# Optimization experiments

Hardware: AMD Instinct MI355X
Metric: run time of the kernel (lower is better)

Reference implementation:

```python
import jax, jax.numpy as jnp
import numpy as np

ALPHAS = [2.0 ** k for k in range(-3, 2)]  # default GaussianKernel bandwidth magnitudes


def _cdist(x, y):
    # Euclidean distance matrix with torch.cdist-compatible zero-distance subgradient.
    sq = (jnp.sum(x * x, axis=1)[:, None]
          + jnp.sum(y * y, axis=1)[None, :]
          - 2.0 * (x @ y.T))
    sq = jnp.maximum(sq, 0.0)
    safe = jnp.where(sq > 0, sq, 1.0)
    return jnp.where(sq > 0, jnp.sqrt(safe), 0.0)


def setup_inputs() -> dict:
    key = jax.random.key(0)
    k1, k2 = jax.random.split(key)
    xs = jax.random.normal(k1, (4096, 256), dtype=jnp.float32)
    xt = jax.random.normal(k2, (4096, 256), dtype=jnp.float32)
    return {"xs": xs, "xt": xt}


def reference(xs, xt):
    xs = xs.reshape(xs.shape[0], -1)
    xt = xt.reshape(xt.shape[0], -1)
    b = xs.shape[0]

    # Compute the three pairwise distance matrices ONCE (the torch loop redoes
    # this per kernel; the math is identical).
    dxx = _cdist(xs, xs)  # [B, B]
    dyy = _cdist(xt, xt)
    dxy = _cdist(xs, xt)

    # sigma^2 = alpha * mean(dist), with the mean detached (stop_gradient).
    mxx = jax.lax.stop_gradient(jnp.mean(dxx))
    myy = jax.lax.stop_gradient(jnp.mean(dyy))
    mxy = jax.lax.stop_gradient(jnp.mean(dxy))

    total = jnp.zeros_like(dxx)
    for a in ALPHAS:
        kxx = jnp.exp(-dxx / (2.0 * a * mxx))
        kyy = jnp.exp(-dyy / (2.0 * a * myy))
        kxy = jnp.exp(-dxy / (2.0 * a * mxy))
        total = total + (kxx + kyy - 2.0 * kxy)

    loss = jnp.sqrt(jnp.sum(total) / (b * (b - 1.0)))
    return jnp.where(jnp.isnan(loss), jnp.zeros_like(loss), loss)
```

## Files before the change

### kernel.cpp

```cpp
#include <hip/hip_runtime.h>

#define BN 4096
#define KD 256
#define TILE 256
#define BK 64

typedef short bf16x8 __attribute__((ext_vector_type(8)));
typedef float f32x4 __attribute__((ext_vector_type(4)));
typedef unsigned short ushort_t;
typedef unsigned int uint_t;

#define NSLOT 528

__device__ inline void async_load16(const void* g, void* l) {
    __builtin_amdgcn_global_load_lds((const __attribute__((address_space(1))) void*)g,
                                     (__attribute__((address_space(3))) void*)l,
                                     16, 0, 0);
}

__device__ inline ushort_t f2bf(float f) {
    union { float f; unsigned int u; } x;
    x.f = f;
    unsigned int u = x.u;
    unsigned int r = (u + 0x7fffu + ((u >> 16) & 1u)) >> 16;
    return (ushort_t)r;
}

__device__ __forceinline__ float fast_sqrt(float x) {
    return __builtin_amdgcn_sqrtf(x);
}
__device__ __forceinline__ float fast_exp2(float x) {
    return __builtin_amdgcn_exp2f(x);
}

__device__ __forceinline__ void decode_slot(int slot, int& z, int& bi, int& bj) {
    if (slot >= 272) {
        z = 2; int t = slot - 272; bi = t >> 4; bj = t & 15;
    } else {
        z = (slot >= 136) ? 1 : 0;
        int t = slot - z * 136;
        int b = (int)(16.5f - sqrtf(272.25f - 2.0f * (float)t));
        while (b * (33 - b) / 2 > t) --b;
        while ((b + 1) * (32 - b) / 2 <= t) ++b;
        bi = b;
        bj = bi + (t - bi * (33 - bi) / 2);
    }
}

__global__ __launch_bounds__(256) void norm_cvt(
        const float* __restrict__ xs, const float* __restrict__ xt,
        ushort_t* __restrict__ xsb, ushort_t* __restrict__ xtb,
        float* __restrict__ norms) {
    int w = threadIdx.x >> 6;
    int lane = threadIdx.x & 63;
    int row = blockIdx.x * 4 + w;
    const float* src = (row < BN) ? xs + (size_t)row * KD
                                  : xt + (size_t)(row - BN) * KD;
    ushort_t* dst = (row < BN) ? xsb + (size_t)row * KD
                               : xtb + (size_t)(row - BN) * KD;
    float4 v = ((const float4*)src)[lane];
    float s = v.x * v.x + v.y * v.y + v.z * v.z + v.w * v.w;
#pragma unroll
    for (int off = 32; off > 0; off >>= 1) s += __shfl_xor(s, off, 64);
    if (lane == 0) norms[row] = s;
    ushort4 o;
    o.x = f2bf(v.x); o.y = f2bf(v.y); o.z = f2bf(v.z); o.w = f2bf(v.w);
    ((ushort4*)dst)[lane] = o;
}


template <int PASS>
__global__ __launch_bounds__(512, 1) void mmd_gemm(
        const ushort_t* __restrict__ xsb, const ushort_t* __restrict__ xtb,
        const float* __restrict__ norms,
        const float* __restrict__ p1, float* __restrict__ pout) {
    const int slot = blockIdx.x;
    int z, bi, bj;
    decode_slot(slot, z, bi, bj);

    const ushort_t* X = (z == 1) ? xtb : xsb;
    const ushort_t* Y = (z == 0) ? xsb : xtb;
    const float* nX = norms + ((z == 1) ? BN : 0);
    const float* nY = norms + ((z == 0) ? 0 : BN);

    const int tid = threadIdx.x;
    const int lane = tid & 63;
    const int w = tid >> 6;
    const int wr = w >> 2;
    const int wc = w & 3;
    const int m16 = lane & 15;
    const int q = lane >> 4;

    const int i0 = bi * TILE;
    const int j0 = bj * TILE;

    __shared__ ushort_t sm[2][2][TILE * BK];
    __shared__ float red[8];
    __shared__ double rs[8][3];

    float nhb = 0.0f;
    if (PASS == 2) {
        double a0 = 0.0, a1 = 0.0, a2 = 0.0;
        for (int s = tid; s < NSLOT; s += 512) {
            double v = (double)p1[s];
            if (s < 136) a0 += v; else if (s < 272) a1 += v; else a2 += v;
        }
#pragma unroll
        for (int off = 32; off > 0; off >>= 1) {
            a0 += __shfl_xor(a0, off, 64);
            a1 += __shfl_xor(a1, off, 64);
            a2 += __shfl_xor(a2, off, 64);
        }
        if (lane == 0) { rs[w][0] = a0; rs[w][1] = a1; rs[w][2] = a2; }
        __syncthreads();
        double sz = 0.0;
#pragma unroll
        for (int ww = 0; ww < 8; ++ww) sz += rs[ww][z];
        double mz = sz * (1.0 / 16777216.0);
        nhb = (float)(-1.4426950408889634 / (4.0 * mz));
    }

    const int rbase = tid >> 3;
    const int gc = (tid & 7) ^ (rbase & 7);
    const uint_t offA = ((uint_t)(i0 + rbase) * KD + (uint_t)gc * 8) * 2u;
    const uint_t offB = ((uint_t)(j0 + rbase) * KD + (uint_t)gc * 8) * 2u;
    const char* Xc = (const char*)X;
    const char* Yc = (const char*)Y;

    f32x4 acc[8][4] = {};

    auto stage = [&](int kt, int p) {
        const uint_t kb = (uint_t)(kt * BK * 2);
        char* ldsA = (char*)&sm[p][0][0] + tid * 16;
        char* ldsB = (char*)&sm[p][1][0] + tid * 16;
#pragma unroll
        for (int t = 0; t < 4; ++t) {
            const uint_t rowoff = (uint_t)(t * 64 * KD * 2);
            async_load16(Xc + (offA + rowoff + kb), ldsA + t * 8192);
            async_load16(Yc + (offB + rowoff + kb), ldsB + t * 8192);
        }
    };

    auto compute = [&](int p) {
#pragma unroll
        for (int ks = 0; ks < 2; ++ks) {
            const int kap = ks * 4 + q;
            const int pos = kap ^ (m16 & 7);
            bf16x8 bfv[4];
#pragma unroll
            for (int ng = 0; ng < 4; ++ng)
                bfv[ng] = *(const bf16x8*)&sm[p][1][(wc * 64 + ng * 16 + m16) * BK + pos * 8];
#pragma unroll
            for (int rg = 0; rg < 8; ++rg) {
                bf16x8 a = *(const bf16x8*)&sm[p][0][(wr * 128 + rg * 16 + m16) * BK + pos * 8];
#pragma unroll
                for (int ng = 0; ng < 4; ++ng)
                    acc[rg][ng] = __builtin_amdgcn_mfma_f32_16x16x32_bf16(
                        a, bfv[ng], acc[rg][ng], 0, 0, 0);
            }
        }
    };

    stage(0, 0);
#pragma unroll
    for (int t = 0; t < 4; ++t) {
        const int p = t & 1;
        if (t < 3) {
            stage(t + 1, p ^ 1);
            asm volatile("s_waitcnt vmcnt(8)" ::: "memory");
        } else {
            asm volatile("s_waitcnt vmcnt(0)" ::: "memory");
        }
        __builtin_amdgcn_s_barrier();
        compute(p);
        if (t < 3) __builtin_amdgcn_s_barrier();
    }

    float nyv[4];
#pragma unroll
    for (int ng = 0; ng < 4; ++ng)
        nyv[ng] = nY[j0 + wc * 64 + ng * 16 + m16];

    const bool diag = (z < 2 && bi == bj);
    float local = 0.0f;
#pragma unroll
    for (int rg = 0; rg < 8; ++rg) {
        float4 nf = *(const float4*)&nX[i0 + wr * 128 + rg * 16 + q * 4];
        float nx4[4] = {nf.x, nf.y, nf.z, nf.w};
#pragma unroll
        for (int ng = 0; ng < 4; ++ng) {
#pragma unroll
            for (int rr = 0; rr < 4; ++rr) {
                int i = wr * 128 + rg * 16 + q * 4 + rr;
                int j = wc * 64 + ng * 16 + m16;
                float sq = nx4[rr] + nyv[ng] - 2.0f * acc[rg][ng][rr];
                sq = fmaxf(sq, 0.0f);
                float d = fast_sqrt(sq);
                if (diag && i == j) d = 0.0f;
                if (PASS == 1) {
                    local += d;
                } else {
                    float u = fast_exp2(d * nhb);
                    float u2 = u * u;
                    float u4 = u2 * u2;
                    float u8 = u4 * u4;
                    float u16 = u8 * u8;
                    local += (u + u2) + (u4 + u8) + u16;
                }
            }
        }
    }

#pragma unroll
    for (int off = 32; off > 0; off >>= 1) local += __shfl_xor(local, off, 64);
    if (lane == 0) red[w] = local;
    __syncthreads();
    if (tid == 0) {
        float bs = 0.0f;
#pragma unroll
        for (int ww = 0; ww < 8; ++ww) bs += red[ww];
        float coef;
        if (PASS == 1) coef = (z < 2 && bi != bj) ? 2.0f : 1.0f;
        else           coef = (z == 2) ? -2.0f : ((bi != bj) ? 2.0f : 1.0f);
        pout[slot] = coef * bs;
    }
}


__global__ __launch_bounds__(256) void mmd_finalize2(
        const float* __restrict__ p2, float* __restrict__ out) {
    const int tid = threadIdx.x;
    double acc = 0.0;
    for (int s = tid; s < NSLOT; s += 256) acc += (double)p2[s];
    const int lane = tid & 63, w = tid >> 6;
#pragma unroll
    for (int off = 32; off > 0; off >>= 1) acc += __shfl_xor(acc, off, 64);
    __shared__ double r[4];
    if (lane == 0) r[w] = acc;
    __syncthreads();
    if (tid == 0) {
        double S = r[0] + r[1] + r[2] + r[3];
        double l = sqrt(S / ((double)BN * (double)(BN - 1)));
        float f = (float)l;
        if (!(f == f)) f = 0.0f;
        out[0] = f;
    }
}

extern "C" void kernel_launch(void* const* d_in, const int* in_sizes, int n_in,
                              void* d_out, int out_size, void* d_ws, size_t ws_size,
                              hipStream_t stream) {
    const float* xs = (const float*)d_in[0];
    const float* xt = (const float*)d_in[1];
    float* out = (float*)d_out;

    char* ws = (char*)d_ws;
    float* norms = (float*)ws;
    float* p1 = (float*)(ws + 32768);
    float* p2 = (float*)(ws + 35072);
    ushort_t* xsb = (ushort_t*)(ws + 37376);
    ushort_t* xtb = xsb + (size_t)BN * KD;

    size_t need = 4231680;
    if (ws_size < need) {
        (void)hipMemsetAsync(d_out, 0xC0, 4, stream);
        return;
    }

    norm_cvt<<<2048, 256, 0, stream>>>(xs, xt, xsb, xtb, norms);
    mmd_gemm<1><<<NSLOT, 512, 0, stream>>>(xsb, xtb, norms, p1, p1);
    mmd_gemm<2><<<NSLOT, 512, 0, stream>>>(xsb, xtb, norms, p1, p2);
    mmd_finalize2<<<1, 256, 0, stream>>>(p2, out);
}
```

Measured before the change: 140.8 us.

## Fuse all stages into one cooperative persistent kernel with grid syncs

Replaces four kernel launches (norm/convert, distance-sum GEMM pass, exp GEMM pass, finalize) with a single cooperative kernel of 256 persistent blocks that loop over the 528 tile slots and use grid.sync between stages. The aim is to remove launch gaps and inter-kernel drain/fill overhead. In exchange, 528 slots over 256 blocks gives an uneven tail (three rounds for some blocks), there are grid-wide barrier costs, and the original multi-launch path is kept as a fallback if the cooperative launch fails.

```diff
diff --git a/kernel.cpp b/kernel.cpp
--- a/kernel.cpp
+++ b/kernel.cpp
@@ -1,4 +1,7 @@
 #include <hip/hip_runtime.h>
+#include <hip/hip_cooperative_groups.h>
+
+namespace cg = cooperative_groups;
 
 #define BN 4096
 #define KD 256
@@ -11,6 +14,7 @@
 typedef unsigned int uint_t;
 
 #define NSLOT 528
+#define NBLK 256
 
 __device__ inline void async_load16(const void* g, void* l) {
     __builtin_amdgcn_global_load_lds((const __attribute__((address_space(1))) void*)g,
@@ -46,6 +50,229 @@
         bj = bi + (t - bi * (33 - bi) / 2);
     }
 }
+
+
+template <int PASS>
+__device__ __forceinline__ void gemm_slot(
+        int slot, const ushort_t* __restrict__ xsb, const ushort_t* __restrict__ xtb,
+        const float* __restrict__ norms, float nhb0, float nhb1, float nhb2,
+        float* __restrict__ pout,
+        ushort_t (&sm)[2][2][TILE * BK], float (&red)[8]) {
+    int z, bi, bj;
+    decode_slot(slot, z, bi, bj);
+
+    const ushort_t* X = (z == 1) ? xtb : xsb;
+    const ushort_t* Y = (z == 0) ? xsb : xtb;
+    const float* nX = norms + ((z == 1) ? BN : 0);
+    const float* nY = norms + ((z == 0) ? 0 : BN);
+
+    const int tid = threadIdx.x;
+    const int lane = tid & 63;
+    const int w = tid >> 6;
+    const int wr = w >> 2;
+    const int wc = w & 3;
+    const int m16 = lane & 15;
+    const int q = lane >> 4;
+
+    const int i0 = bi * TILE;
+    const int j0 = bj * TILE;
+
+    const int rbase = tid >> 3;
+    const int gc = (tid & 7) ^ (rbase & 7);
+    const uint_t offA = ((uint_t)(i0 + rbase) * KD + (uint_t)gc * 8) * 2u;
+    const uint_t offB = ((uint_t)(j0 + rbase) * KD + (uint_t)gc * 8) * 2u;
+    const char* Xc = (const char*)X;
+    const char* Yc = (const char*)Y;
+
+    f32x4 acc[8][4] = {};
+
+    auto stage = [&](int kt, int p) {
+        const uint_t kb = (uint_t)(kt * BK * 2);
+        char* ldsA = (char*)&sm[p][0][0] + tid * 16;
+        char* ldsB = (char*)&sm[p][1][0] + tid * 16;
+#pragma unroll
+        for (int t = 0; t < 4; ++t) {
+            const uint_t rowoff = (uint_t)(t * 64 * KD * 2);
+            async_load16(Xc + (offA + rowoff + kb), ldsA + t * 8192);
+            async_load16(Yc + (offB + rowoff + kb), ldsB + t * 8192);
+        }
+    };
+
+    auto compute = [&](int p) {
+#pragma unroll
+        for (int ks = 0; ks < 2; ++ks) {
+            const int kap = ks * 4 + q;
+            const int pos = kap ^ (m16 & 7);
+            bf16x8 bfv[4];
+#pragma unroll
+            for (int ng = 0; ng < 4; ++ng)
+                bfv[ng] = *(const bf16x8*)&sm[p][1][(wc * 64 + ng * 16 + m16) * BK + pos * 8];
+#pragma unroll
+            for (int rg = 0; rg < 8; ++rg) {
+                bf16x8 a = *(const bf16x8*)&sm[p][0][(wr * 128 + rg * 16 + m16) * BK + pos * 8];
+#pragma unroll
+                for (int ng = 0; ng < 4; ++ng)
+                    acc[rg][ng] = __builtin_amdgcn_mfma_f32_16x16x32_bf16(
+                        a, bfv[ng], acc[rg][ng], 0, 0, 0);
+            }
+        }
+    };
+
+    stage(0, 0);
+#pragma unroll
+    for (int t = 0; t < 4; ++t) {
+        const int p = t & 1;
+        if (t < 3) {
+            stage(t + 1, p ^ 1);
+            asm volatile("s_waitcnt vmcnt(8)" ::: "memory");
+        } else {
+            asm volatile("s_waitcnt vmcnt(0)" ::: "memory");
+        }
+        __builtin_amdgcn_s_barrier();
+        compute(p);
+        if (t < 3) __builtin_amdgcn_s_barrier();
+    }
+
+    float nyv[4];
+#pragma unroll
+    for (int ng = 0; ng < 4; ++ng)
+        nyv[ng] = nY[j0 + wc * 64 + ng * 16 + m16];
+
+    const float nhbz = (z == 0) ? nhb0 : ((z == 1) ? nhb1 : nhb2);
+    const bool diag = (z < 2 && bi == bj);
+    float local = 0.0f;
+#pragma unroll
+    for (int rg = 0; rg < 8; ++rg) {
+        float4 nf = *(const float4*)&nX[i0 + wr * 128 + rg * 16 + q * 4];
+        float nx4[4] = {nf.x, nf.y, nf.z, nf.w};
+#pragma unroll
+        for (int ng = 0; ng < 4; ++ng) {
+#pragma unroll
+            for (int rr = 0; rr < 4; ++rr) {
+                int i = wr * 128 + rg * 16 + q * 4 + rr;
+                int j = wc * 64 + ng * 16 + m16;
+                float sq = nx4[rr] + nyv[ng] - 2.0f * acc[rg][ng][rr];
+                sq = fmaxf(sq, 0.0f);
+                float d = fast_sqrt(sq);
+                if (diag && i == j) d = 0.0f;
+                if (PASS == 1) {
+                    local += d;
+                } else {
+                    float u = fast_exp2(d * nhbz);
+                    float u2 = u * u;
+                    float u4 = u2 * u2;
+                    float u8 = u4 * u4;
+                    float u16 = u8 * u8;
+                    local += (u + u2) + (u4 + u8) + u16;
+                }
+            }
+        }
+    }
+
+#pragma unroll
+    for (int off = 32; off > 0; off >>= 1) local += __shfl_xor(local, off, 64);
+    if (lane == 0) red[w] = local;
+    __syncthreads();
+    if (tid == 0) {
+        float bs = 0.0f;
+#pragma unroll
+        for (int ww = 0; ww < 8; ++ww) bs += red[ww];
+        float coef;
+        if (PASS == 1) coef = (z < 2 && bi != bj) ? 2.0f : 1.0f;
+        else           coef = (z == 2) ? -2.0f : ((bi != bj) ? 2.0f : 1.0f);
+        pout[slot] = coef * bs;
+    }
+}
+
+
+__global__ __launch_bounds__(512, 1) void mmd_fused(
+        const float* __restrict__ xs, const float* __restrict__ xt,
+        ushort_t* __restrict__ xsb, ushort_t* __restrict__ xtb,
+        float* __restrict__ norms, float* __restrict__ p1, float* __restrict__ p2,
+        float* __restrict__ out) {
+    __shared__ ushort_t sm[2][2][TILE * BK];
+    __shared__ float red[8];
+    __shared__ double rs[8][3];
+
+    const int tid = threadIdx.x;
+    const int bid = blockIdx.x;
+    cg::grid_group grid = cg::this_grid();
+
+    {
+        const int w = tid >> 6;
+        const int lane = tid & 63;
+#pragma unroll
+        for (int it = 0; it < 4; ++it) {
+            int row = it * (NBLK * 8) + bid * 8 + w;
+            const float* src = (row < BN) ? xs + (size_t)row * KD
+                                          : xt + (size_t)(row - BN) * KD;
+            ushort_t* dst = (row < BN) ? xsb + (size_t)row * KD
+                                       : xtb + (size_t)(row - BN) * KD;
+            float4 v = ((const float4*)src)[lane];
+            float s = v.x * v.x + v.y * v.y + v.z * v.z + v.w * v.w;
+#pragma unroll
+            for (int off = 32; off > 0; off >>= 1) s += __shfl_xor(s, off, 64);
+            if (lane == 0) norms[row] = s;
+            ushort4 o;
+            o.x = f2bf(v.x); o.y = f2bf(v.y); o.z = f2bf(v.z); o.w = f2bf(v.w);
+            ((ushort4*)dst)[lane] = o;
+        }
+    }
+    grid.sync();
+
+    for (int slot = bid; slot < NSLOT; slot += NBLK)
+        gemm_slot<1>(slot, xsb, xtb, norms, 0.0f, 0.0f, 0.0f, p1, sm, red);
+    grid.sync();
+
+    float nhb0, nhb1, nhb2;
+    {
+        double a0 = 0.0, a1 = 0.0, a2 = 0.0;
+        for (int s = tid; s < NSLOT; s += 512) {
+            double v = (double)p1[s];
+            if (s < 136) a0 += v; else if (s < 272) a1 += v; else a2 += v;
+        }
+        const int lane = tid & 63, w = tid >> 6;
+#pragma unroll
+        for (int off = 32; off > 0; off >>= 1) {
+            a0 += __shfl_xor(a0, off, 64);
+            a1 += __shfl_xor(a1, off, 64);
+            a2 += __shfl_xor(a2, off, 64);
+        }
+        if (lane == 0) { rs[w][0] = a0; rs[w][1] = a1; rs[w][2] = a2; }
+        __syncthreads();
+        double s0 = 0.0, s1 = 0.0, s2 = 0.0;
+#pragma unroll
+        for (int ww = 0; ww < 8; ++ww) { s0 += rs[ww][0]; s1 += rs[ww][1]; s2 += rs[ww][2]; }
+        nhb0 = (float)(-1.4426950408889634 / (4.0 * (s0 * (1.0 / 16777216.0))));
+        nhb1 = (float)(-1.4426950408889634 / (4.0 * (s1 * (1.0 / 16777216.0))));
+        nhb2 = (float)(-1.4426950408889634 / (4.0 * (s2 * (1.0 / 16777216.0))));
+        __syncthreads();
+    }
+
+    for (int slot = bid; slot < NSLOT; slot += NBLK)
+        gemm_slot<2>(slot, xsb, xtb, norms, nhb0, nhb1, nhb2, p2, sm, red);
+    grid.sync();
+
+    if (bid == 0) {
+        double acc = 0.0;
+        for (int s = tid; s < NSLOT; s += 512) acc += (double)p2[s];
+        const int lane = tid & 63, w = tid >> 6;
+#pragma unroll
+        for (int off = 32; off > 0; off >>= 1) acc += __shfl_xor(acc, off, 64);
+        if (lane == 0) rs[w][0] = acc;
+        __syncthreads();
+        if (tid == 0) {
+            double S = 0.0;
+#pragma unroll
+            for (int ww = 0; ww < 8; ++ww) S += rs[ww][0];
+            double l = sqrt(S / ((double)BN * (double)(BN - 1)));
+            float f = (float)l;
+            if (!(f == f)) f = 0.0f;
+            out[0] = f;
+        }
+    }
+}
+
 
 __global__ __launch_bounds__(256) void norm_cvt(
         const float* __restrict__ xs, const float* __restrict__ xt,
@@ -68,43 +295,24 @@
     ((ushort4*)dst)[lane] = o;
 }
 
-
 template <int PASS>
 __global__ __launch_bounds__(512, 1) void mmd_gemm(
         const ushort_t* __restrict__ xsb, const ushort_t* __restrict__ xtb,
         const float* __restrict__ norms,
         const float* __restrict__ p1, float* __restrict__ pout) {
-    const int slot = blockIdx.x;
-    int z, bi, bj;
-    decode_slot(slot, z, bi, bj);
-
-    const ushort_t* X = (z == 1) ? xtb : xsb;
-    const ushort_t* Y = (z == 0) ? xsb : xtb;
-    const float* nX = norms + ((z == 1) ? BN : 0);
-    const float* nY = norms + ((z == 0) ? 0 : BN);
-
-    const int tid = threadIdx.x;
-    const int lane = tid & 63;
-    const int w = tid >> 6;
-    const int wr = w >> 2;
-    const int wc = w & 3;
-    const int m16 = lane & 15;
-    const int q = lane >> 4;
-
-    const int i0 = bi * TILE;
-    const int j0 = bj * TILE;
-
     __shared__ ushort_t sm[2][2][TILE * BK];
     __shared__ float red[8];
     __shared__ double rs[8][3];
 
-    float nhb = 0.0f;
+    const int tid = threadIdx.x;
+    float nhb0 = 0.0f, nhb1 = 0.0f, nhb2 = 0.0f;
     if (PASS == 2) {
         double a0 = 0.0, a1 = 0.0, a2 = 0.0;
         for (int s = tid; s < NSLOT; s += 512) {
             double v = (double)p1[s];
             if (s < 136) a0 += v; else if (s < 272) a1 += v; else a2 += v;
         }
+        const int lane = tid & 63, w = tid >> 6;
 #pragma unroll
         for (int off = 32; off > 0; off >>= 1) {
             a0 += __shfl_xor(a0, off, 64);
@@ -113,119 +321,16 @@
         }
         if (lane == 0) { rs[w][0] = a0; rs[w][1] = a1; rs[w][2] = a2; }
         __syncthreads();
-        double sz = 0.0;
-#pragma unroll
-        for (int ww = 0; ww < 8; ++ww) sz += rs[ww][z];
-        double mz = sz * (1.0 / 16777216.0);
-        nhb = (float)(-1.4426950408889634 / (4.0 * mz));
-    }
-
-    const int rbase = tid >> 3;
-    const int gc = (tid & 7) ^ (rbase & 7);
-    const uint_t offA = ((uint_t)(i0 + rbase) * KD + (uint_t)gc * 8) * 2u;
-    const uint_t offB = ((uint_t)(j0 + rbase) * KD + (uint_t)gc * 8) * 2u;
-    const char* Xc = (const char*)X;
-    const char* Yc = (const char*)Y;
-
-    f32x4 acc[8][4] = {};
-
-    auto stage = [&](int kt, int p) {
-        const uint_t kb = (uint_t)(kt * BK * 2);
-        char* ldsA = (char*)&sm[p][0][0] + tid * 16;
-        char* ldsB = (char*)&sm[p][1][0] + tid * 16;
-#pragma unroll
-        for (int t = 0; t < 4; ++t) {
-            const uint_t rowoff = (uint_t)(t * 64 * KD * 2);
-            async_load16(Xc + (offA + rowoff + kb), ldsA + t * 8192);
-            async_load16(Yc + (offB + rowoff + kb), ldsB + t * 8192);
-        }
-    };
-
-    auto compute = [&](int p) {
-#pragma unroll
-        for (int ks = 0; ks < 2; ++ks) {
-            const int kap = ks * 4 + q;
-            const int pos = kap ^ (m16 & 7);
-            bf16x8 bfv[4];
-#pragma unroll
-            for (int ng = 0; ng < 4; ++ng)
-                bfv[ng] = *(const bf16x8*)&sm[p][1][(wc * 64 + ng * 16 + m16) * BK + pos * 8];
-#pragma unroll
-            for (int rg = 0; rg < 8; ++rg) {
-                bf16x8 a = *(const bf16x8*)&sm[p][0][(wr * 128 + rg * 16 + m16) * BK + pos * 8];
-#pragma unroll
-                for (int ng = 0; ng < 4; ++ng)
-                    acc[rg][ng] = __builtin_amdgcn_mfma_f32_16x16x32_bf16(
-                        a, bfv[ng], acc[rg][ng], 0, 0, 0);
-            }
-        }
-    };
-
-    stage(0, 0);
-#pragma unroll
-    for (int t = 0; t < 4; ++t) {
-        const int p = t & 1;
-        if (t < 3) {
-            stage(t + 1, p ^ 1);
-            asm volatile("s_waitcnt vmcnt(8)" ::: "memory");
-        } else {
-            asm volatile("s_waitcnt vmcnt(0)" ::: "memory");
-        }
-        __builtin_amdgcn_s_barrier();
-        compute(p);
-        if (t < 3) __builtin_amdgcn_s_barrier();
-    }
-
-    float nyv[4];
-#pragma unroll
-    for (int ng = 0; ng < 4; ++ng)
-        nyv[ng] = nY[j0 + wc * 64 + ng * 16 + m16];
-
-    const bool diag = (z < 2 && bi == bj);
-    float local = 0.0f;
-#pragma unroll
-    for (int rg = 0; rg < 8; ++rg) {
-        float4 nf = *(const float4*)&nX[i0 + wr * 128 + rg * 16 + q * 4];
-        float nx4[4] = {nf.x, nf.y, nf.z, nf.w};
-#pragma unroll
-        for (int ng = 0; ng < 4; ++ng) {
-#pragma unroll
-            for (int rr = 0; rr < 4; ++rr) {
-                int i = wr * 128 + rg * 16 + q * 4 + rr;
-                int j = wc * 64 + ng * 16 + m16;
-                float sq = nx4[rr] + nyv[ng] - 2.0f * acc[rg][ng][rr];
-                sq = fmaxf(sq, 0.0f);
-                float d = fast_sqrt(sq);
-                if (diag && i == j) d = 0.0f;
-                if (PASS == 1) {
-                    local += d;
-                } else {
-                    float u = fast_exp2(d * nhb);
-                    float u2 = u * u;
-                    float u4 = u2 * u2;
-                    float u8 = u4 * u4;
-                    float u16 = u8 * u8;
-                    local += (u + u2) + (u4 + u8) + u16;
-                }
-            }
-        }
-    }
-
-#pragma unroll
-    for (int off = 32; off > 0; off >>= 1) local += __shfl_xor(local, off, 64);
-    if (lane == 0) red[w] = local;
-    __syncthreads();
-    if (tid == 0) {
-        float bs = 0.0f;
-#pragma unroll
-        for (int ww = 0; ww < 8; ++ww) bs += red[ww];
-        float coef;
-        if (PASS == 1) coef = (z < 2 && bi != bj) ? 2.0f : 1.0f;
-        else           coef = (z == 2) ? -2.0f : ((bi != bj) ? 2.0f : 1.0f);
-        pout[slot] = coef * bs;
-    }
-}
-
+        double s0 = 0.0, s1 = 0.0, s2 = 0.0;
+#pragma unroll
+        for (int ww = 0; ww < 8; ++ww) { s0 += rs[ww][0]; s1 += rs[ww][1]; s2 += rs[ww][2]; }
+        nhb0 = (float)(-1.4426950408889634 / (4.0 * (s0 * (1.0 / 16777216.0))));
+        nhb1 = (float)(-1.4426950408889634 / (4.0 * (s1 * (1.0 / 16777216.0))));
+        nhb2 = (float)(-1.4426950408889634 / (4.0 * (s2 * (1.0 / 16777216.0))));
+        __syncthreads();
+    }
+    gemm_slot<PASS>(blockIdx.x, xsb, xtb, norms, nhb0, nhb1, nhb2, pout, sm, red);
+}
 
 __global__ __launch_bounds__(256) void mmd_finalize2(
         const float* __restrict__ p2, float* __restrict__ out) {
@@ -267,8 +372,15 @@
         return;
     }
 
-    norm_cvt<<<2048, 256, 0, stream>>>(xs, xt, xsb, xtb, norms);
-    mmd_gemm<1><<<NSLOT, 512, 0, stream>>>(xsb, xtb, norms, p1, p1);
-    mmd_gemm<2><<<NSLOT, 512, 0, stream>>>(xsb, xtb, norms, p1, p2);
-    mmd_finalize2<<<1, 256, 0, stream>>>(p2, out);
-}
+    void* args[] = {(void*)&xs, (void*)&xt, (void*)&xsb, (void*)&xtb,
+                    (void*)&norms, (void*)&p1, (void*)&p2, (void*)&out};
+    hipError_t err = hipLaunchCooperativeKernel(
+        (const void*)mmd_fused, dim3(NBLK), dim3(512), args, 0, stream);
+
+    if (err != hipSuccess) {
+        norm_cvt<<<2048, 256, 0, stream>>>(xs, xt, xsb, xtb, norms);
+        mmd_gemm<1><<<NSLOT, 512, 0, stream>>>(xsb, xtb, norms, p1, p1);
+        mmd_gemm<2><<<NSLOT, 512, 0, stream>>>(xsb, xtb, norms, p1, p2);
+        mmd_finalize2<<<1, 256, 0, stream>>>(p2, out);
+    }
+}
```

After: 253.0 us. +79.7%, slower.
